# Kernel optimization log

Hardware: AMD Instinct MI355X
Metric: run time of the kernel (lower is better)

Reference implementation:

```python
import jax, jax.numpy as jnp
import numpy as np

N = 50000      # nodes
E = 800000     # edges
IN_CH = 32
H = 64         # hidden_channels
OUT_CH = 16
L = 4          # num_layers
EPS = 1e-7     # GENConv message eps
LN_EPS = 1e-5


def _lin(key, fan_in, fan_out):
    kw, kb = jax.random.split(key)
    s = 1.0 / np.sqrt(fan_in)
    W = jax.random.uniform(kw, (fan_in, fan_out), jnp.float32, -s, s)
    b = jax.random.uniform(kb, (fan_out,), jnp.float32, -s, s)
    return W, b


def setup_inputs() -> dict:
    key = jax.random.key(0)
    ks = jax.random.split(key, 8)
    x = jax.random.normal(ks[0], (N, IN_CH), jnp.float32)
    edge_index = jax.random.randint(ks[1], (2, E), 0, N, dtype=jnp.int32)
    node_W, node_b = _lin(ks[2], IN_CH, H)
    W1, b1, W2, b2 = [], [], [], []
    for i in range(L):
        w1, bb1 = _lin(jax.random.fold_in(ks[3], i), H, 2 * H)
        w2, bb2 = _lin(jax.random.fold_in(ks[4], i), 2 * H, H)
        W1.append(w1); b1.append(bb1); W2.append(w2); b2.append(bb2)
    inp = {
        "x": x,
        "node_W": node_W, "node_b": node_b,
        "W1": jnp.stack(W1), "b1": jnp.stack(b1),          # [L,H,2H],[L,2H]
        "mlp_ln_g": jnp.ones((L, 2 * H), jnp.float32),      # LayerNorm inside GENConv MLP
        "mlp_ln_b": jnp.zeros((L, 2 * H), jnp.float32),
        "W2": jnp.stack(W2), "b2": jnp.stack(b2),          # [L,2H,H],[L,H]
        "t": jnp.ones((L,), jnp.float32),                   # learnable softmax temperature
        "ln_g": jnp.ones((L, H), jnp.float32),              # DeepGCNLayer LayerNorms
        "ln_b": jnp.zeros((L, H), jnp.float32),
        "edge_index": edge_index,
    }
    gW, gb = _lin(ks[5], H, OUT_CH)
    nW, nb = _lin(ks[6], H, OUT_CH + 1)
    inp.update({"g_W": gW, "g_b": gb, "n_W": nW, "n_b": nb})
    return inp


def _layer_norm(h, g, b):
    mu = h.mean(-1, keepdims=True)
    var = ((h - mu) ** 2).mean(-1, keepdims=True)
    return (h - mu) * jax.lax.rsqrt(var + LN_EPS) * g + b


def _gen_conv(h, src, dst, W1, b1, lg, lb, W2, b2, t):
    # message: relu(x_j) + eps  -> [E, H]
    m = jax.nn.relu(h[src]) + EPS
    # per-destination, per-channel scatter softmax with temperature t
    z = t * m
    zmax = jax.ops.segment_max(z, dst, num_segments=N)
    zmax = jnp.where(jnp.isfinite(zmax), zmax, 0.0)  # empty segments -> -inf
    a = jnp.exp(z - zmax[dst])
    denom = jax.ops.segment_sum(a, dst, num_segments=N)
    agg = jax.ops.segment_sum(m * a, dst, num_segments=N) / jnp.maximum(denom, EPS)
    out = agg + h  # root add
    # MLP [H, 2H, H] with LayerNorm + ReLU between
    u = jax.nn.relu(_layer_norm(out @ W1 + b1, lg, lb))
    return u @ W2 + b2


def reference(x, node_W, node_b, W1, b1, mlp_ln_g, mlp_ln_b, W2, b2, t,
              ln_g, ln_b, g_W, g_b, n_W, n_b, edge_index):
    src, dst = edge_index[0], edge_index[1]
    h = x @ node_W + node_b  # node encoder
    # first layer: conv only
    h = _gen_conv(h, src, dst, W1[0], b1[0], mlp_ln_g[0], mlp_ln_b[0], W2[0], b2[0], t[0])
    # remaining res+ blocks: x + conv(relu(norm(x)))  (dropout identity in eval)
    for i in range(1, L):
        y = jax.nn.relu(_layer_norm(h, ln_g[i], ln_b[i]))
        h = h + _gen_conv(y, src, dst, W1[i], b1[i], mlp_ln_g[i], mlp_ln_b[i], W2[i], b2[i], t[i])
    h = jax.nn.relu(_layer_norm(h, ln_g[0], ln_b[0]))
    g_out = jnp.max(h @ g_W + g_b, axis=0)   # batch=None -> global max over nodes
    n_out = h @ n_W + n_b
    return g_out, n_out
```

## Files before the change

### kernel.cpp

```cpp
#include <hip/hip_runtime.h>

#define NN 50000
#define NE 800000
#define INC 32
#define HH 64
#define H2 128
#define OC 16
#define ON 17
#define NL 4
#define MEPS 1e-7f
#define LNE 1e-5f
#define SCAN_BLOCKS 196
#define NOB ((NN + 63) / 64)

typedef __attribute__((ext_vector_type(8))) short bf16x8;
typedef __attribute__((ext_vector_type(4))) float f32x4;

__device__ __forceinline__ unsigned short f2b(float x) {
    unsigned b = __float_as_uint(x);
    b += 0x7FFFu + ((b >> 16) & 1u);
    return (unsigned short)(b >> 16);
}
__device__ __forceinline__ float b2f(unsigned short u) {
    return __uint_as_float(((unsigned)u) << 16);
}

__global__ __launch_bounds__(256) void k_hist2(const int* __restrict__ dst, int* __restrict__ counts,
                                               int* __restrict__ rank) {
    int e = blockIdx.x * 256 + threadIdx.x;
    if (e < NE) rank[e] = atomicAdd(&counts[dst[e]], 1);
}

__global__ __launch_bounds__(256) void k_scan1(const int* __restrict__ counts,
                                               int* __restrict__ incl, int* __restrict__ bsums) {
    __shared__ int s[256];
    int t = threadIdx.x;
    int i = blockIdx.x * 256 + t;
    int v = (i < NN) ? counts[i] : 0;
    s[t] = v;
    __syncthreads();
    for (int off = 1; off < 256; off <<= 1) {
        int x = (t >= off) ? s[t - off] : 0;
        __syncthreads();
        s[t] += x;
        __syncthreads();
    }
    if (i < NN) incl[i] = s[t];
    if (t == 255) bsums[blockIdx.x] = s[255];
}

__global__ __launch_bounds__(256) void k_scan2(int* __restrict__ bsums) {
    __shared__ int s[256];
    int t = threadIdx.x;
    int v = (t < SCAN_BLOCKS) ? bsums[t] : 0;
    s[t] = v;
    __syncthreads();
    for (int off = 1; off < 256; off <<= 1) {
        int x = (t >= off) ? s[t - off] : 0;
        __syncthreads();
        s[t] += x;
        __syncthreads();
    }
    if (t < SCAN_BLOCKS) bsums[t] = s[t] - v;
}

__global__ __launch_bounds__(256) void k_scan3(const int* __restrict__ counts,
                                               int* __restrict__ rowst, const int* __restrict__ bsums,
                                               int2* __restrict__ meta) {
    int i = blockIdx.x * 256 + threadIdx.x;
    if (i < NN) {
        int st = rowst[i] - counts[i] + bsums[blockIdx.x];
        rowst[i] = st;
        meta[i] = make_int2(st, counts[i]);
    }
}

__global__ __launch_bounds__(256) void k_scatter2(const int* __restrict__ src, const int* __restrict__ dst,
                                                  const int* __restrict__ rank, const int* __restrict__ rowst,
                                                  int* __restrict__ ssrc) {
    int e = blockIdx.x * 256 + threadIdx.x;
    if (e < NE) ssrc[rowst[dst[e]] + rank[e]] = src[e];
}

__global__ __launch_bounds__(256) void k_wprep(const float* __restrict__ W1, const float* __restrict__ W2,
                                               const float* __restrict__ nW, const float* __restrict__ gW,
                                               const float* __restrict__ nbp, const float* __restrict__ gb,
                                               unsigned short* __restrict__ w1h, unsigned short* __restrict__ w1l,
                                               unsigned short* __restrict__ w2h, unsigned short* __restrict__ w2l,
                                               unsigned short* __restrict__ whh, unsigned short* __restrict__ whl,
                                               float* __restrict__ bc) {
    int i = blockIdx.x * 256 + threadIdx.x;
    if (i < 48 * 64) {
        int j = i >> 6, k = i & 63;
        float v = 0.f;
        if (j < ON) v = nW[k * ON + j];
        else if (j < 33) v = gW[k * OC + (j - ON)];
        unsigned short hi = f2b(v);
        whh[i] = hi;
        whl[i] = f2b(v - b2f(hi));
    }
    if (i < 48) bc[i] = (i < ON) ? nbp[i] : ((i < 33) ? gb[i - ON] : 0.f);
    if (i >= NL * H2 * HH) return;
    int l = i / (H2 * HH), r = i % (H2 * HH);
    {
        int c = r / HH, k = r % HH;
        float v = W1[(size_t)l * HH * H2 + (size_t)k * H2 + c];
        unsigned short hi = f2b(v);
        w1h[i] = hi;
        w1l[i] = f2b(v - b2f(hi));
    }
    {
        int c = r / H2, k = r % H2;
        float v = W2[(size_t)l * H2 * HH + (size_t)k * HH + c];
        unsigned short hi = f2b(v);
        w2h[i] = hi;
        w2l[i] = f2b(v - b2f(hi));
    }
}

__global__ __launch_bounds__(256) void k_encoder(const float* __restrict__ x, const float* __restrict__ W,
                                                 const float* __restrict__ b, float* __restrict__ h,
                                                 unsigned short* __restrict__ hbf) {
    __shared__ float Ws[INC * HH];
    __shared__ float bs[HH];
    int tid = threadIdx.x;
    for (int i = tid; i < INC * HH; i += 256) Ws[i] = W[i];
    if (tid < HH) bs[tid] = b[tid];
    __syncthreads();
    int wid = tid >> 6, lane = tid & 63;
    int n = blockIdx.x * 4 + wid;
    if (n >= NN) return;
    float v = (lane < INC) ? x[(size_t)n * INC + lane] : 0.f;
    float acc = bs[lane];
    #pragma unroll
    for (int k = 0; k < INC; ++k)
        acc += __shfl(v, k) * Ws[k * HH + lane];
    h[(size_t)n * HH + lane] = acc;
    hbf[(size_t)n * HH + lane] = f2b(acc);
}

__global__ __launch_bounds__(256) void k_agg(const float* __restrict__ y,
                                             const unsigned short* __restrict__ ybf,
                                             const int2* __restrict__ meta,
                                             const int* __restrict__ ssrc,
                                             const float* __restrict__ tp,
                                             unsigned short* __restrict__ agh,
                                             unsigned short* __restrict__ agl) {
    int tid = threadIdx.x;
    int w = tid >> 6, lane = tid & 63;
    int half = lane >> 5;
    int l = lane & 31;
    int col = l;
    int n = blockIdx.x * 8 + w * 2 + half;
    bool valid = n < NN;
    float tval = *tp;
    int2 m = valid ? meta[n] : make_int2(0, 0);
    int start = m.x, deg = m.y;

    int dA = __shfl(deg, 0), dB = __shfl(deg, 32);
    int dmax = max(dA, dB);

    float Sa0 = 0.f, Sm0 = 0.f, Sa1 = 0.f, Sm1 = 0.f;
    for (int win = 0; win < dmax; win += 64) {
        int rem = dmax - win;
        int wcnt = min(64, rem);
        int idxLo = (win + l < deg) ? ssrc[start + win + l] : 0;
        int idxHi = (win + 32 + l < deg) ? ssrc[start + win + 32 + l] : 0;
        for (int e0 = 0; e0 < wcnt; e0 += 8) {
            float c0[8], c1[8];
            int ev[8];
            #pragma unroll
            for (int i = 0; i < 8; ++i) {
                int e = e0 + i;
                ev[i] = win + e;
                int sel = (e < 32) ? idxLo : idxHi;
                int s = __shfl(sel, (lane & 32) | (e & 31));
                unsigned v = *(const unsigned*)(ybf + (size_t)s * HH + col * 2);
                c0[i] = b2f((unsigned short)(v & 0xffffu));
                c1[i] = b2f((unsigned short)(v >> 16));
            }
            #pragma unroll
            for (int i = 0; i < 8; ++i) {
                bool ok = ev[i] < deg;
                float m0 = fmaxf(c0[i], 0.f) + MEPS;
                float m1 = fmaxf(c1[i], 0.f) + MEPS;
                float a0 = ok ? __expf(tval * m0) : 0.f;
                float a1 = ok ? __expf(tval * m1) : 0.f;
                Sa0 += a0; Sm0 += m0 * a0;
                Sa1 += a1; Sm1 += m1 * a1;
            }
        }
    }
    if (!valid) return;
    float agg0 = Sm0 / fmaxf(Sa0, MEPS);
    float agg1 = Sm1 / fmaxf(Sa1, MEPS);
    float2 yv = *(const float2*)(y + (size_t)n * HH + col * 2);
    float av0 = agg0 + yv.x;
    float av1 = agg1 + yv.y;
    unsigned short h0 = f2b(av0), h1 = f2b(av1);
    ushort2 ph = {h0, h1};
    ushort2 pl = {f2b(av0 - b2f(h0)), f2b(av1 - b2f(h1))};
    *(ushort2*)(agh + (size_t)n * HH + col * 2) = ph;
    *(ushort2*)(agl + (size_t)n * HH + col * 2) = pl;
}

__global__ __launch_bounds__(512, 4) void k_mlp(
    const unsigned short* __restrict__ agh, const unsigned short* __restrict__ agl,
    const unsigned short* __restrict__ w1h, const unsigned short* __restrict__ w1l,
    const float* __restrict__ b1,
    const float* __restrict__ mlg, const float* __restrict__ mlb,
    const unsigned short* __restrict__ w2h, const unsigned short* __restrict__ w2l,
    const float* __restrict__ b2,
    const float* __restrict__ hres, float* __restrict__ hout,
    const float* __restrict__ lng1, const float* __restrict__ lnb1,
    float* __restrict__ y, unsigned short* __restrict__ ybf)
{
    __shared__ __align__(16) unsigned short W1S[2 * 128 * 72];
    __shared__ __align__(16) unsigned short W2hS[64 * 136];
    __shared__ __align__(16) unsigned short W2lS[64 * 136];
    int tid = threadIdx.x;
    int w = tid >> 6, lane = tid & 63;
    int nl = lane & 15, g = lane >> 4;
    int node = blockIdx.x * 128 + w * 16 + nl;
    bool valid = node < NN;

    bf16x8 bAh[2], bAl[2];
    {
        bf16x8 z = {0, 0, 0, 0, 0, 0, 0, 0};
        if (valid) {
            const unsigned short* rp = agh + (size_t)node * HH + g * 8;
            bAh[0] = *(const bf16x8*)rp;
            bAh[1] = *(const bf16x8*)(rp + 32);
            const unsigned short* rq = agl + (size_t)node * HH + g * 8;
            bAl[0] = *(const bf16x8*)rq;
            bAl[1] = *(const bf16x8*)(rq + 32);
        } else {
            bAh[0] = z; bAh[1] = z; bAl[0] = z; bAl[1] = z;
        }
    }

    #pragma unroll
    for (int it = 0; it < 2; ++it) {
        int c = tid + it * 512;
        int row = c >> 3, col = (c & 7) << 3;
        float4 vh = *(const float4*)(w1h + c * 8);
        float4 vl = *(const float4*)(w1l + c * 8);
        *(float4*)&W1S[row * 72 + col] = vh;
        *(float4*)&W1S[9216 + row * 72 + col] = vl;
    }
    #pragma unroll
    for (int it = 0; it < 2; ++it) {
        int c = tid + it * 512;
        int row = c >> 4, col = (c & 15) << 3;
        float4 vh = *(const float4*)(w2h + c * 8);
        float4 vl = *(const float4*)(w2l + c * 8);
        *(float4*)&W2hS[row * 136 + col] = vh;
        *(float4*)&W2lS[row * 136 + col] = vl;
    }
    __syncthreads();

    f32x4 accU[8];
    #pragma unroll
    for (int t = 0; t < 8; ++t) {
        int uc = t * 16 + g * 4;
        float4 bb = *(const float4*)(b1 + uc);
        f32x4 a = {bb.x, bb.y, bb.z, bb.w};
        #pragma unroll
        for (int kc = 0; kc < 2; ++kc) {
            int wo = (t * 16 + nl) * 72 + kc * 32 + g * 8;
            bf16x8 ah = *(const bf16x8*)&W1S[wo];
            bf16x8 al = *(const bf16x8*)&W1S[9216 + wo];
            a = __builtin_amdgcn_mfma_f32_16x16x32_bf16(ah, bAh[kc], a, 0, 0, 0);
            a = __builtin_amdgcn_mfma_f32_16x16x32_bf16(al, bAh[kc], a, 0, 0, 0);
            a = __builtin_amdgcn_mfma_f32_16x16x32_bf16(ah, bAl[kc], a, 0, 0, 0);
        }
        accU[t] = a;
    }

    float s = 0.f, sq = 0.f;
    #pragma unroll
    for (int t = 0; t < 8; ++t) {
        #pragma unroll
        for (int j = 0; j < 4; ++j) { float v = accU[t][j]; s += v; sq += v * v; }
    }
    s += __shfl_xor(s, 16); sq += __shfl_xor(sq, 16);
    s += __shfl_xor(s, 32); sq += __shfl_xor(sq, 32);
    float mu = s * (1.f / 128.f);
    float var = sq * (1.f / 128.f) - mu * mu;
    float rs = rsqrtf(fmaxf(var, 0.f) + LNE);

    __syncthreads();
    unsigned short* myUt = W1S + w * (16 * 136);

    #pragma unroll
    for (int t = 0; t < 8; ++t) {
        int uc = t * 16 + g * 4;
        float4 gg = *(const float4*)(mlg + uc);
        float4 bb = *(const float4*)(mlb + uc);
        ushort4 pk;
        pk.x = f2b(fmaxf((accU[t][0] - mu) * rs * gg.x + bb.x, 0.f));
        pk.y = f2b(fmaxf((accU[t][1] - mu) * rs * gg.y + bb.y, 0.f));
        pk.z = f2b(fmaxf((accU[t][2] - mu) * rs * gg.z + bb.z, 0.f));
        pk.w = f2b(fmaxf((accU[t][3] - mu) * rs * gg.w + bb.w, 0.f));
        *(ushort4*)(&myUt[nl * 136 + uc]) = pk;
    }
    asm volatile("s_waitcnt lgkmcnt(0)" ::: "memory");

    bf16x8 bB[4];
    #pragma unroll
    for (int kc = 0; kc < 4; ++kc)
        bB[kc] = *(const bf16x8*)(&myUt[nl * 136 + kc * 32 + g * 8]);

    f32x4 accO[4];
    #pragma unroll
    for (int ot = 0; ot < 4; ++ot) {
        int oc = ot * 16 + g * 4;
        float4 bb = *(const float4*)(b2 + oc);
        f32x4 a = {bb.x, bb.y, bb.z, bb.w};
        #pragma unroll
        for (int kc = 0; kc < 4; ++kc) {
            int wo = (ot * 16 + nl) * 136 + kc * 32 + g * 8;
            bf16x8 ah = *(const bf16x8*)&W2hS[wo];
            bf16x8 al = *(const bf16x8*)&W2lS[wo];
            a = __builtin_amdgcn_mfma_f32_16x16x32_bf16(ah, bB[kc], a, 0, 0, 0);
            a = __builtin_amdgcn_mfma_f32_16x16x32_bf16(al, bB[kc], a, 0, 0, 0);
        }
        accO[ot] = a;
    }

    float4 oo[4];
    #pragma unroll
    for (int ot = 0; ot < 4; ++ot) {
        int oc = ot * 16 + g * 4;
        float4 o;
        o.x = accO[ot][0]; o.y = accO[ot][1]; o.z = accO[ot][2]; o.w = accO[ot][3];
        if (valid) {
            if (hres) {
                float4 hr = *(const float4*)(hres + (size_t)node * HH + oc);
                o.x += hr.x; o.y += hr.y; o.z += hr.z; o.w += hr.w;
            }
            *(float4*)(hout + (size_t)node * HH + oc) = o;
        }
        oo[ot] = o;
    }
    if (!lng1) return;

    float s2 = 0.f, sq2 = 0.f;
    #pragma unroll
    for (int ot = 0; ot < 4; ++ot) {
        s2 += oo[ot].x + oo[ot].y + oo[ot].z + oo[ot].w;
        sq2 += oo[ot].x * oo[ot].x + oo[ot].y * oo[ot].y
             + oo[ot].z * oo[ot].z + oo[ot].w * oo[ot].w;
    }
    s2 += __shfl_xor(s2, 16); sq2 += __shfl_xor(sq2, 16);
    s2 += __shfl_xor(s2, 32); sq2 += __shfl_xor(sq2, 32);
    float mu2 = s2 * (1.f / 64.f);
    float var2 = sq2 * (1.f / 64.f) - mu2 * mu2;
    float rs2 = rsqrtf(fmaxf(var2, 0.f) + LNE);
    #pragma unroll
    for (int ot = 0; ot < 4; ++ot) {
        int oc = ot * 16 + g * 4;
        float4 gg = *(const float4*)(lng1 + oc);
        float4 bb = *(const float4*)(lnb1 + oc);
        float4 v;
        v.x = fmaxf((oo[ot].x - mu2) * rs2 * gg.x + bb.x, 0.f);
        v.y = fmaxf((oo[ot].y - mu2) * rs2 * gg.y + bb.y, 0.f);
        v.z = fmaxf((oo[ot].z - mu2) * rs2 * gg.z + bb.z, 0.f);
        v.w = fmaxf((oo[ot].w - mu2) * rs2 * gg.w + bb.w, 0.f);
        if (valid) {
            *(float4*)(y + (size_t)node * HH + oc) = v;
            ushort4 p;
            p.x = f2b(v.x); p.y = f2b(v.y); p.z = f2b(v.z); p.w = f2b(v.w);
            *(ushort4*)(ybf + (size_t)node * HH + oc) = p;
        }
    }
}

__global__ __launch_bounds__(256) void k_outg(const float* __restrict__ h,
                                              const float* __restrict__ lng, const float* __restrict__ lnb,
                                              const unsigned short* __restrict__ whh,
                                              const unsigned short* __restrict__ whl,
                                              const float* __restrict__ bc,
                                              float* __restrict__ dout, float* __restrict__ gmax) {
    __shared__ float smax[4][16];
    int tid = threadIdx.x;
    int w = tid >> 6, lane = tid & 63;
    int nl = lane & 15, g = lane >> 4;
    int node = blockIdx.x * 64 + w * 16 + nl;
    bool valid = node < NN;

    float hv[16];
    if (valid) {
        const float* hp = h + (size_t)node * HH;
        float4 a0 = *(const float4*)(hp + g * 8);
        float4 a1 = *(const float4*)(hp + g * 8 + 4);
        float4 a2 = *(const float4*)(hp + 32 + g * 8);
        float4 a3 = *(const float4*)(hp + 32 + g * 8 + 4);
        hv[0] = a0.x; hv[1] = a0.y; hv[2] = a0.z; hv[3] = a0.w;
        hv[4] = a1.x; hv[5] = a1.y; hv[6] = a1.z; hv[7] = a1.w;
        hv[8] = a2.x; hv[9] = a2.y; hv[10] = a2.z; hv[11] = a2.w;
        hv[12] = a3.x; hv[13] = a3.y; hv[14] = a3.z; hv[15] = a3.w;
    } else {
        #pragma unroll
        for (int i = 0; i < 16; ++i) hv[i] = 0.f;
    }

    float s = 0.f, sq = 0.f;
    #pragma unroll
    for (int i = 0; i < 16; ++i) { s += hv[i]; sq += hv[i] * hv[i]; }
    s += __shfl_xor(s, 16); sq += __shfl_xor(sq, 16);
    s += __shfl_xor(s, 32); sq += __shfl_xor(sq, 32);
    float mu = s * (1.f / 64.f);
    float var = sq * (1.f / 64.f) - mu * mu;
    float rs = rsqrtf(fmaxf(var, 0.f) + LNE);

    union { bf16x8 v; unsigned short u[8]; } Bh[2], Bl[2];
    #pragma unroll
    for (int kc = 0; kc < 2; ++kc) {
        int cb = kc * 32 + g * 8;
        float4 g0 = *(const float4*)(lng + cb);
        float4 g1 = *(const float4*)(lng + cb + 4);
        float4 b0 = *(const float4*)(lnb + cb);
        float4 b1v = *(const float4*)(lnb + cb + 4);
        float gv[8] = {g0.x, g0.y, g0.z, g0.w, g1.x, g1.y, g1.z, g1.w};
        float bv[8] = {b0.x, b0.y, b0.z, b0.w, b1v.x, b1v.y, b1v.z, b1v.w};
        #pragma unroll
        for (int e = 0; e < 8; ++e) {
            float v = fmaxf((hv[kc * 8 + e] - mu) * rs * gv[e] + bv[e], 0.f);
            unsigned short hi = f2b(v);
            Bh[kc].u[e] = hi;
            Bl[kc].u[e] = f2b(v - b2f(hi));
        }
    }

    f32x4 acc[3];
    #pragma unroll
    for (int t = 0; t < 3; ++t) {
        int j0 = t * 16 + g * 4;
        float4 bb = *(const float4*)(bc + j0);
        f32x4 a = {bb.x, bb.y, bb.z, bb.w};
        #pragma unroll
        for (int kc = 0; kc < 2; ++kc) {
            size_t wo = (size_t)(t * 16 + nl) * 64 + kc * 32 + g * 8;
            bf16x8 ah = *(const bf16x8*)(whh + wo);
            bf16x8 al = *(const bf16x8*)(whl + wo);
            a = __builtin_amdgcn_mfma_f32_16x16x32_bf16(ah, Bh[kc].v, a, 0, 0, 0);
            a = __builtin_amdgcn_mfma_f32_16x16x32_bf16(al, Bh[kc].v, a, 0, 0, 0);
            a = __builtin_amdgcn_mfma_f32_16x16x32_bf16(ah, Bl[kc].v, a, 0, 0, 0);
        }
        acc[t] = a;
    }

    #pragma unroll
    for (int t = 0; t < 3; ++t) {
        #pragma unroll
        for (int reg = 0; reg < 4; ++reg) {
            int j = t * 16 + g * 4 + reg;
            float val = acc[t][reg];
            if (j < ON) {
                if (valid) dout[OC + (size_t)node * ON + j] = val;
            } else if (j < 33) {
                float gv = valid ? val : -INFINITY;
                #pragma unroll
                for (int m = 1; m < 16; m <<= 1) gv = fmaxf(gv, __shfl_xor(gv, m));
                if (nl == 0) smax[w][j - ON] = gv;
            }
        }
    }
    __syncthreads();
    if (tid < 16) {
        float m = fmaxf(fmaxf(smax[0][tid], smax[1][tid]),
                        fmaxf(smax[2][tid], smax[3][tid]));
        gmax[(size_t)blockIdx.x * 16 + tid] = m;
    }
}

__global__ void k_gdec(const float* __restrict__ gmax, float* __restrict__ dout) {
    int lane = threadIdx.x & 63;
    int ch = lane & 15, grp = lane >> 4;
    float m = -INFINITY;
    for (int b = grp; b < NOB; b += 4) m = fmaxf(m, gmax[(size_t)b * 16 + ch]);
    m = fmaxf(m, __shfl_xor(m, 16));
    m = fmaxf(m, __shfl_xor(m, 32));
    if (lane < 16) dout[ch] = m;
}

extern "C" void kernel_launch(void* const* d_in, const int* in_sizes, int n_in,
                              void* d_out, int out_size, void* d_ws, size_t ws_size,
                              hipStream_t stream) {
    const float* x     = (const float*)d_in[0];
    const float* nodeW = (const float*)d_in[1];
    const float* nodeB = (const float*)d_in[2];
    const float* W1    = (const float*)d_in[3];
    const float* b1    = (const float*)d_in[4];
    const float* mlg   = (const float*)d_in[5];
    const float* mlb   = (const float*)d_in[6];
    const float* W2    = (const float*)d_in[7];
    const float* b2    = (const float*)d_in[8];
    const float* tt    = (const float*)d_in[9];
    const float* lng   = (const float*)d_in[10];
    const float* lnb   = (const float*)d_in[11];
    const int*   ei    = (const int*)d_in[12];
    const float* gW    = (const float*)d_in[13];
    const float* gb    = (const float*)d_in[14];
    const float* nW    = (const float*)d_in[15];
    const float* nbp   = (const float*)d_in[16];
    float* out = (float*)d_out;

    char* ws = (char*)d_ws;
    size_t off = 0;
    auto alloc = [&](size_t bytes) -> void* {
        void* p = ws + off;
        off = (off + bytes + 255) & ~(size_t)255;
        return p;
    };
    int* counts    = (int*)alloc((size_t)NN * 4);
    size_t zero_end = off;
    float* gmax = (float*)alloc((size_t)NOB * 16 * 4);
    int* bsums = (int*)alloc(1024);
    int* rowst = (int*)alloc((size_t)NN * 4);
    int2* meta = (int2*)alloc((size_t)NN * 8);
    int* ssrc  = (int*)alloc((size_t)NE * 4);
    float* h   = (float*)alloc((size_t)NN * HH * 4);
    float* y   = (float*)alloc((size_t)NN * HH * 4);
    unsigned short* agh = (unsigned short*)alloc((size_t)NN * HH * 2);
    unsigned short* agl = (unsigned short*)alloc((size_t)NN * HH * 2);
    unsigned short* ybf = (unsigned short*)alloc((size_t)NN * HH * 2);
    unsigned short* w1h = (unsigned short*)alloc((size_t)NL * H2 * HH * 2);
    unsigned short* w1l = (unsigned short*)alloc((size_t)NL * H2 * HH * 2);
    unsigned short* w2h = (unsigned short*)alloc((size_t)NL * H2 * HH * 2);
    unsigned short* w2l = (unsigned short*)alloc((size_t)NL * H2 * HH * 2);
    unsigned short* whh = (unsigned short*)alloc((size_t)48 * 64 * 2);
    unsigned short* whl = (unsigned short*)alloc((size_t)48 * 64 * 2);
    float* bc = (float*)alloc(48 * 4);
    int* rank = (int*)agh;

    const int* esrc = ei;
    const int* edst = ei + NE;

    hipMemsetAsync(d_ws, 0, zero_end, stream);

    k_wprep<<<(NL * H2 * HH + 255) / 256, 256, 0, stream>>>(W1, W2, nW, gW, nbp, gb,
                                                            w1h, w1l, w2h, w2l, whh, whl, bc);
    k_hist2<<<(NE + 255) / 256, 256, 0, stream>>>(edst, counts, rank);
    k_scan1<<<SCAN_BLOCKS, 256, 0, stream>>>(counts, rowst, bsums);
    k_scan2<<<1, 256, 0, stream>>>(bsums);
    k_scan3<<<SCAN_BLOCKS, 256, 0, stream>>>(counts, rowst, bsums, meta);
    k_scatter2<<<(NE + 255) / 256, 256, 0, stream>>>(esrc, edst, rank, rowst, ssrc);
    k_encoder<<<(NN + 3) / 4, 256, 0, stream>>>(x, nodeW, nodeB, h, ybf);

    for (int l = 0; l < NL; ++l) {
        const float* yin = (l == 0) ? h : y;
        k_agg<<<(NN + 7) / 8, 256, 0, stream>>>(yin, ybf, meta, ssrc, tt + l, agh, agl);
        const float* ln1g = (l < NL - 1) ? (lng + (size_t)(l + 1) * HH) : nullptr;
        const float* ln1b = (l < NL - 1) ? (lnb + (size_t)(l + 1) * HH) : nullptr;
        k_mlp<<<(NN + 127) / 128, 512, 0, stream>>>(agh, agl,
                                                    w1h + (size_t)l * H2 * HH, w1l + (size_t)l * H2 * HH,
                                                    b1 + (size_t)l * H2,
                                                    mlg + (size_t)l * H2, mlb + (size_t)l * H2,
                                                    w2h + (size_t)l * H2 * HH, w2l + (size_t)l * H2 * HH,
                                                    b2 + (size_t)l * HH,
                                                    (l == 0) ? (const float*)nullptr : h, h,
                                                    ln1g, ln1b, y, ybf);
    }
    k_outg<<<NOB, 256, 0, stream>>>(h, lng, lnb, whh, whl, bc, out, gmax);
    k_gdec<<<1, 64, 0, stream>>>(gmax, out);
}
```

Baseline: 402.4 us.

## Fuse aggregation, MLP and output head into one per-layer kernel

Merges the weight prep, degree histogram and node encoder into a single multi-role launch, combines scan phases 2 and 3, and fuses the per-layer softmax aggregation into the MLP kernel. The aggregated features now stay in shared memory instead of going to global hi/lo buffers, and the final LayerNorm plus output head runs in the last layer's kernel. The bf16 feature buffer is double-buffered because each layer reads one copy while writing the next. This removes several launches and a global round trip per layer. In exchange, each MLP block of 128 nodes now does the irregular gather itself, which may lower overlap and occupancy and leave the block load uneven.

```diff
diff --git a/kernel.cpp b/kernel.cpp
--- a/kernel.cpp
+++ b/kernel.cpp
@@ -11,7 +11,10 @@
 #define MEPS 1e-7f
 #define LNE 1e-5f
 #define SCAN_BLOCKS 196
-#define NOB ((NN + 63) / 64)
+#define NLB ((NN + 127) / 128)
+#define NBW ((NL * H2 * HH + 255) / 256)
+#define NBH ((NE + 255) / 256)
+#define NBE ((NN + 3) / 4)
 
 typedef __attribute__((ext_vector_type(8))) short bf16x8;
 typedef __attribute__((ext_vector_type(4))) float f32x4;
@@ -25,10 +28,70 @@
     return __uint_as_float(((unsigned)u) << 16);
 }
 
-__global__ __launch_bounds__(256) void k_hist2(const int* __restrict__ dst, int* __restrict__ counts,
-                                               int* __restrict__ rank) {
-    int e = blockIdx.x * 256 + threadIdx.x;
-    if (e < NE) rank[e] = atomicAdd(&counts[dst[e]], 1);
+__global__ __launch_bounds__(256) void k_pre(
+    const float* __restrict__ W1, const float* __restrict__ W2,
+    const float* __restrict__ nW, const float* __restrict__ gW,
+    const float* __restrict__ nbp, const float* __restrict__ gb,
+    unsigned short* __restrict__ w1h, unsigned short* __restrict__ w1l,
+    unsigned short* __restrict__ w2h, unsigned short* __restrict__ w2l,
+    unsigned short* __restrict__ whh, unsigned short* __restrict__ whl,
+    float* __restrict__ bc,
+    const int* __restrict__ edst, int* __restrict__ counts, int* __restrict__ rank,
+    const float* __restrict__ x, const float* __restrict__ nodeW,
+    const float* __restrict__ nodeB, float* __restrict__ h,
+    unsigned short* __restrict__ hbf)
+{
+    __shared__ float Ws[INC * HH];
+    __shared__ float bs[HH];
+    int bid = blockIdx.x, tid = threadIdx.x;
+    if (bid < NBW) {
+        int i = bid * 256 + tid;
+        if (i < 48 * 64) {
+            int j = i >> 6, k = i & 63;
+            float v = 0.f;
+            if (j < ON) v = nW[k * ON + j];
+            else if (j < 33) v = gW[k * OC + (j - ON)];
+            unsigned short hi = f2b(v);
+            whh[i] = hi;
+            whl[i] = f2b(v - b2f(hi));
+        }
+        if (i < 48) bc[i] = (i < ON) ? nbp[i] : ((i < 33) ? gb[i - ON] : 0.f);
+        if (i >= NL * H2 * HH) return;
+        int l = i / (H2 * HH), r = i % (H2 * HH);
+        {
+            int c = r / HH, k = r % HH;
+            float v = W1[(size_t)l * HH * H2 + (size_t)k * H2 + c];
+            unsigned short hi = f2b(v);
+            w1h[i] = hi;
+            w1l[i] = f2b(v - b2f(hi));
+        }
+        {
+            int c = r / H2, k = r % H2;
+            float v = W2[(size_t)l * H2 * HH + (size_t)k * HH + c];
+            unsigned short hi = f2b(v);
+            w2h[i] = hi;
+            w2l[i] = f2b(v - b2f(hi));
+        }
+        return;
+    }
+    if (bid < NBW + NBH) {
+        int e = (bid - NBW) * 256 + tid;
+        if (e < NE) rank[e] = atomicAdd(&counts[edst[e]], 1);
+        return;
+    }
+    for (int i = tid; i < INC * HH; i += 256) Ws[i] = nodeW[i];
+    if (tid < HH) bs[tid] = nodeB[tid];
+    __syncthreads();
+    int wid = tid >> 6, lane = tid & 63;
+    int n = (bid - NBW - NBH) * 4 + wid;
+    if (n >= NN) return;
+    float v = (lane < INC) ? x[(size_t)n * INC + lane] : 0.f;
+    float acc = bs[lane];
+    #pragma unroll
+    for (int k = 0; k < INC; ++k)
+        acc += __shfl(v, k) * Ws[k * HH + lane];
+    h[(size_t)n * HH + lane] = acc;
+    hbf[(size_t)n * HH + lane] = f2b(acc);
 }
 
 __global__ __launch_bounds__(256) void k_scan1(const int* __restrict__ counts,
@@ -49,7 +112,9 @@
     if (t == 255) bsums[blockIdx.x] = s[255];
 }
 
-__global__ __launch_bounds__(256) void k_scan2(int* __restrict__ bsums) {
+__global__ __launch_bounds__(256) void k_scan23(const int* __restrict__ counts,
+                                                int* __restrict__ rowst, const int* __restrict__ bsums,
+                                                int2* __restrict__ meta) {
     __shared__ int s[256];
     int t = threadIdx.x;
     int v = (t < SCAN_BLOCKS) ? bsums[t] : 0;
@@ -61,15 +126,14 @@
         s[t] += x;
         __syncthreads();
     }
-    if (t < SCAN_BLOCKS) bsums[t] = s[t] - v;
-}
-
-__global__ __launch_bounds__(256) void k_scan3(const int* __restrict__ counts,
-                                               int* __restrict__ rowst, const int* __restrict__ bsums,
-                                               int2* __restrict__ meta) {
-    int i = blockIdx.x * 256 + threadIdx.x;
+    int ex = s[t] - v;
+    __syncthreads();
+    s[t] = ex;
+    __syncthreads();
+    int pref = s[blockIdx.x];
+    int i = blockIdx.x * 256 + t;
     if (i < NN) {
-        int st = rowst[i] - counts[i] + bsums[blockIdx.x];
+        int st = rowst[i] - counts[i] + pref;
         rowst[i] = st;
         meta[i] = make_int2(st, counts[i]);
     }
@@ -82,130 +146,9 @@
     if (e < NE) ssrc[rowst[dst[e]] + rank[e]] = src[e];
 }
 
-__global__ __launch_bounds__(256) void k_wprep(const float* __restrict__ W1, const float* __restrict__ W2,
-                                               const float* __restrict__ nW, const float* __restrict__ gW,
-                                               const float* __restrict__ nbp, const float* __restrict__ gb,
-                                               unsigned short* __restrict__ w1h, unsigned short* __restrict__ w1l,
-                                               unsigned short* __restrict__ w2h, unsigned short* __restrict__ w2l,
-                                               unsigned short* __restrict__ whh, unsigned short* __restrict__ whl,
-                                               float* __restrict__ bc) {
-    int i = blockIdx.x * 256 + threadIdx.x;
-    if (i < 48 * 64) {
-        int j = i >> 6, k = i & 63;
-        float v = 0.f;
-        if (j < ON) v = nW[k * ON + j];
-        else if (j < 33) v = gW[k * OC + (j - ON)];
-        unsigned short hi = f2b(v);
-        whh[i] = hi;
-        whl[i] = f2b(v - b2f(hi));
-    }
-    if (i < 48) bc[i] = (i < ON) ? nbp[i] : ((i < 33) ? gb[i - ON] : 0.f);
-    if (i >= NL * H2 * HH) return;
-    int l = i / (H2 * HH), r = i % (H2 * HH);
-    {
-        int c = r / HH, k = r % HH;
-        float v = W1[(size_t)l * HH * H2 + (size_t)k * H2 + c];
-        unsigned short hi = f2b(v);
-        w1h[i] = hi;
-        w1l[i] = f2b(v - b2f(hi));
-    }
-    {
-        int c = r / H2, k = r % H2;
-        float v = W2[(size_t)l * H2 * HH + (size_t)k * HH + c];
-        unsigned short hi = f2b(v);
-        w2h[i] = hi;
-        w2l[i] = f2b(v - b2f(hi));
-    }
-}
-
-__global__ __launch_bounds__(256) void k_encoder(const float* __restrict__ x, const float* __restrict__ W,
-                                                 const float* __restrict__ b, float* __restrict__ h,
-                                                 unsigned short* __restrict__ hbf) {
-    __shared__ float Ws[INC * HH];
-    __shared__ float bs[HH];
-    int tid = threadIdx.x;
-    for (int i = tid; i < INC * HH; i += 256) Ws[i] = W[i];
-    if (tid < HH) bs[tid] = b[tid];
-    __syncthreads();
-    int wid = tid >> 6, lane = tid & 63;
-    int n = blockIdx.x * 4 + wid;
-    if (n >= NN) return;
-    float v = (lane < INC) ? x[(size_t)n * INC + lane] : 0.f;
-    float acc = bs[lane];
-    #pragma unroll
-    for (int k = 0; k < INC; ++k)
-        acc += __shfl(v, k) * Ws[k * HH + lane];
-    h[(size_t)n * HH + lane] = acc;
-    hbf[(size_t)n * HH + lane] = f2b(acc);
-}
-
-__global__ __launch_bounds__(256) void k_agg(const float* __restrict__ y,
-                                             const unsigned short* __restrict__ ybf,
-                                             const int2* __restrict__ meta,
-                                             const int* __restrict__ ssrc,
-                                             const float* __restrict__ tp,
-                                             unsigned short* __restrict__ agh,
-                                             unsigned short* __restrict__ agl) {
-    int tid = threadIdx.x;
-    int w = tid >> 6, lane = tid & 63;
-    int half = lane >> 5;
-    int l = lane & 31;
-    int col = l;
-    int n = blockIdx.x * 8 + w * 2 + half;
-    bool valid = n < NN;
-    float tval = *tp;
-    int2 m = valid ? meta[n] : make_int2(0, 0);
-    int start = m.x, deg = m.y;
-
-    int dA = __shfl(deg, 0), dB = __shfl(deg, 32);
-    int dmax = max(dA, dB);
-
-    float Sa0 = 0.f, Sm0 = 0.f, Sa1 = 0.f, Sm1 = 0.f;
-    for (int win = 0; win < dmax; win += 64) {
-        int rem = dmax - win;
-        int wcnt = min(64, rem);
-        int idxLo = (win + l < deg) ? ssrc[start + win + l] : 0;
-        int idxHi = (win + 32 + l < deg) ? ssrc[start + win + 32 + l] : 0;
-        for (int e0 = 0; e0 < wcnt; e0 += 8) {
-            float c0[8], c1[8];
-            int ev[8];
-            #pragma unroll
-            for (int i = 0; i < 8; ++i) {
-                int e = e0 + i;
-                ev[i] = win + e;
-                int sel = (e < 32) ? idxLo : idxHi;
-                int s = __shfl(sel, (lane & 32) | (e & 31));
-                unsigned v = *(const unsigned*)(ybf + (size_t)s * HH + col * 2);
-                c0[i] = b2f((unsigned short)(v & 0xffffu));
-                c1[i] = b2f((unsigned short)(v >> 16));
-            }
-            #pragma unroll
-            for (int i = 0; i < 8; ++i) {
-                bool ok = ev[i] < deg;
-                float m0 = fmaxf(c0[i], 0.f) + MEPS;
-                float m1 = fmaxf(c1[i], 0.f) + MEPS;
-                float a0 = ok ? __expf(tval * m0) : 0.f;
-                float a1 = ok ? __expf(tval * m1) : 0.f;
-                Sa0 += a0; Sm0 += m0 * a0;
-                Sa1 += a1; Sm1 += m1 * a1;
-            }
-        }
-    }
-    if (!valid) return;
-    float agg0 = Sm0 / fmaxf(Sa0, MEPS);
-    float agg1 = Sm1 / fmaxf(Sa1, MEPS);
-    float2 yv = *(const float2*)(y + (size_t)n * HH + col * 2);
-    float av0 = agg0 + yv.x;
-    float av1 = agg1 + yv.y;
-    unsigned short h0 = f2b(av0), h1 = f2b(av1);
-    ushort2 ph = {h0, h1};
-    ushort2 pl = {f2b(av0 - b2f(h0)), f2b(av1 - b2f(h1))};
-    *(ushort2*)(agh + (size_t)n * HH + col * 2) = ph;
-    *(ushort2*)(agl + (size_t)n * HH + col * 2) = pl;
-}
-
-__global__ __launch_bounds__(512, 4) void k_mlp(
-    const unsigned short* __restrict__ agh, const unsigned short* __restrict__ agl,
+__global__ __launch_bounds__(512, 4) void k_layer(
+    const float* __restrict__ yin, const unsigned short* __restrict__ ybf_in,
+    const int2* __restrict__ meta, const int* __restrict__ ssrc, const float* __restrict__ tp,
     const unsigned short* __restrict__ w1h, const unsigned short* __restrict__ w1l,
     const float* __restrict__ b1,
     const float* __restrict__ mlg, const float* __restrict__ mlb,
@@ -213,31 +156,25 @@
     const float* __restrict__ b2,
     const float* __restrict__ hres, float* __restrict__ hout,
     const float* __restrict__ lng1, const float* __restrict__ lnb1,
-    float* __restrict__ y, unsigned short* __restrict__ ybf)
+    float* __restrict__ yout, unsigned short* __restrict__ ybf_out,
+    const float* __restrict__ lngF, const float* __restrict__ lnbF,
+    const unsigned short* __restrict__ whh, const unsigned short* __restrict__ whl,
+    const float* __restrict__ bc, float* __restrict__ dout, float* __restrict__ gmax)
 {
-    __shared__ __align__(16) unsigned short W1S[2 * 128 * 72];
-    __shared__ __align__(16) unsigned short W2hS[64 * 136];
-    __shared__ __align__(16) unsigned short W2lS[64 * 136];
+    __shared__ __align__(16) unsigned short R1[2 * 128 * 68];
+    __shared__ __align__(16) unsigned short R2[2 * 128 * 72];
+    __shared__ float smax[8][16];
+    unsigned short* aghS = R1;
+    unsigned short* aglS = R1 + 128 * 68;
+    unsigned short* W2hS = R1;
+    unsigned short* W2lS = R1 + 128 * 68;
+    bool last = (lng1 == nullptr);
     int tid = threadIdx.x;
     int w = tid >> 6, lane = tid & 63;
     int nl = lane & 15, g = lane >> 4;
-    int node = blockIdx.x * 128 + w * 16 + nl;
-    bool valid = node < NN;
-
-    bf16x8 bAh[2], bAl[2];
-    {
-        bf16x8 z = {0, 0, 0, 0, 0, 0, 0, 0};
-        if (valid) {
-            const unsigned short* rp = agh + (size_t)node * HH + g * 8;
-            bAh[0] = *(const bf16x8*)rp;
-            bAh[1] = *(const bf16x8*)(rp + 32);
-            const unsigned short* rq = agl + (size_t)node * HH + g * 8;
-            bAl[0] = *(const bf16x8*)rq;
-            bAl[1] = *(const bf16x8*)(rq + 32);
-        } else {
-            bAh[0] = z; bAh[1] = z; bAl[0] = z; bAl[1] = z;
-        }
-    }
+    int nodeM = blockIdx.x * 128 + w * 16 + nl;
+    bool validM = nodeM < NN;
+    float tval = *tp;
 
     #pragma unroll
     for (int it = 0; it < 2; ++it) {
@@ -245,9 +182,104 @@
         int row = c >> 3, col = (c & 7) << 3;
         float4 vh = *(const float4*)(w1h + c * 8);
         float4 vl = *(const float4*)(w1l + c * 8);
-        *(float4*)&W1S[row * 72 + col] = vh;
-        *(float4*)&W1S[9216 + row * 72 + col] = vl;
-    }
+        *(float4*)&R2[row * 72 + col] = vh;
+        *(float4*)&R2[9216 + row * 72 + col] = vl;
+    }
+
+    {
+        int half = lane >> 5, l = lane & 31;
+        for (int p = 0; p < 8; ++p) {
+            int ln = p * 16 + w * 2 + half;
+            int n = blockIdx.x * 128 + ln;
+            bool valid = n < NN;
+            int2 m = valid ? meta[n] : make_int2(0, 0);
+            int start = m.x, deg = m.y;
+            int dA = __shfl(deg, 0), dB = __shfl(deg, 32);
+            int dmax = max(dA, dB);
+            float Sa0 = 0.f, Sm0 = 0.f, Sa1 = 0.f, Sm1 = 0.f;
+            for (int win = 0; win < dmax; win += 64) {
+                int wcnt = min(64, dmax - win);
+                int idxLo = (win + l < deg) ? ssrc[start + win + l] : 0;
+                int idxHi = (win + 32 + l < deg) ? ssrc[start + win + 32 + l] : 0;
+                for (int e0 = 0; e0 < wcnt; e0 += 8) {
+                    float c0[8], c1[8];
+                    int ev[8];
+                    #pragma unroll
+                    for (int i = 0; i < 8; ++i) {
+                        int e = e0 + i;
+                        ev[i] = win + e;
+                        int sel = (e < 32) ? idxLo : idxHi;
+                        int s = __shfl(sel, (lane & 32) | (e & 31));
+                        unsigned vv = *(const unsigned*)(ybf_in + (size_t)s * HH + l * 2);
+                        c0[i] = b2f((unsigned short)(vv & 0xffffu));
+                        c1[i] = b2f((unsigned short)(vv >> 16));
+                    }
+                    #pragma unroll
+                    for (int i = 0; i < 8; ++i) {
+                        bool ok = ev[i] < deg;
+                        float m0 = fmaxf(c0[i], 0.f) + MEPS;
+                        float m1 = fmaxf(c1[i], 0.f) + MEPS;
+                        float a0 = ok ? __expf(tval * m0) : 0.f;
+                        float a1 = ok ? __expf(tval * m1) : 0.f;
+                        Sa0 += a0; Sm0 += m0 * a0;
+                        Sa1 += a1; Sm1 += m1 * a1;
+                    }
+                }
+            }
+            float av0 = 0.f, av1 = 0.f;
+            if (valid) {
+                float2 yv = *(const float2*)(yin + (size_t)n * HH + l * 2);
+                av0 = Sm0 / fmaxf(Sa0, MEPS) + yv.x;
+                av1 = Sm1 / fmaxf(Sa1, MEPS) + yv.y;
+            }
+            unsigned short h0 = f2b(av0), h1 = f2b(av1);
+            ushort2 ph = {h0, h1};
+            ushort2 pl = {f2b(av0 - b2f(h0)), f2b(av1 - b2f(h1))};
+            *(ushort2*)&aghS[ln * 68 + 2 * l] = ph;
+            *(ushort2*)&aglS[ln * 68 + 2 * l] = pl;
+        }
+    }
+    __syncthreads();
+
+    int lnM = w * 16 + nl;
+    bf16x8 bAh[2], bAl[2];
+    #pragma unroll
+    for (int kc = 0; kc < 2; ++kc) {
+        bAh[kc] = *(const bf16x8*)&aghS[lnM * 68 + kc * 32 + g * 8];
+        bAl[kc] = *(const bf16x8*)&aglS[lnM * 68 + kc * 32 + g * 8];
+    }
+    f32x4 accU[8];
+    #pragma unroll
+    for (int t = 0; t < 8; ++t) {
+        int uc = t * 16 + g * 4;
+        float4 bb = *(const float4*)(b1 + uc);
+        f32x4 a = {bb.x, bb.y, bb.z, bb.w};
+        #pragma unroll
+        for (int kc = 0; kc < 2; ++kc) {
+            int wo = (t * 16 + nl) * 72 + kc * 32 + g * 8;
+            bf16x8 ah = *(const bf16x8*)&R2[wo];
+            bf16x8 al = *(const bf16x8*)&R2[9216 + wo];
+            a = __builtin_amdgcn_mfma_f32_16x16x32_bf16(ah, bAh[kc], a, 0, 0, 0);
+            a = __builtin_amdgcn_mfma_f32_16x16x32_bf16(al, bAh[kc], a, 0, 0, 0);
+            a = __builtin_amdgcn_mfma_f32_16x16x32_bf16(ah, bAl[kc], a, 0, 0, 0);
+        }
+        accU[t] = a;
+    }
+
+    float s = 0.f, sq = 0.f;
+    #pragma unroll
+    for (int t = 0; t < 8; ++t) {
+        #pragma unroll
+        for (int j = 0; j < 4; ++j) { float v = accU[t][j]; s += v; sq += v * v; }
+    }
+    s += __shfl_xor(s, 16); sq += __shfl_xor(sq, 16);
+    s += __shfl_xor(s, 32); sq += __shfl_xor(sq, 32);
+    float mu = s * (1.f / 128.f);
+    float var = sq * (1.f / 128.f) - mu * mu;
+    float rs = rsqrtf(fmaxf(var, 0.f) + LNE);
+
+    __syncthreads();
+
     #pragma unroll
     for (int it = 0; it < 2; ++it) {
         int c = tid + it * 512;
@@ -257,41 +289,7 @@
         *(float4*)&W2hS[row * 136 + col] = vh;
         *(float4*)&W2lS[row * 136 + col] = vl;
     }
-    __syncthreads();
-
-    f32x4 accU[8];
-    #pragma unroll
-    for (int t = 0; t < 8; ++t) {
-        int uc = t * 16 + g * 4;
-        float4 bb = *(const float4*)(b1 + uc);
-        f32x4 a = {bb.x, bb.y, bb.z, bb.w};
-        #pragma unroll
-        for (int kc = 0; kc < 2; ++kc) {
-            int wo = (t * 16 + nl) * 72 + kc * 32 + g * 8;
-            bf16x8 ah = *(const bf16x8*)&W1S[wo];
-            bf16x8 al = *(const bf16x8*)&W1S[9216 + wo];
-            a = __builtin_amdgcn_mfma_f32_16x16x32_bf16(ah, bAh[kc], a, 0, 0, 0);
-            a = __builtin_amdgcn_mfma_f32_16x16x32_bf16(al, bAh[kc], a, 0, 0, 0);
-            a = __builtin_amdgcn_mfma_f32_16x16x32_bf16(ah, bAl[kc], a, 0, 0, 0);
-        }
-        accU[t] = a;
-    }
-
-    float s = 0.f, sq = 0.f;
-    #pragma unroll
-    for (int t = 0; t < 8; ++t) {
-        #pragma unroll
-        for (int j = 0; j < 4; ++j) { float v = accU[t][j]; s += v; sq += v * v; }
-    }
-    s += __shfl_xor(s, 16); sq += __shfl_xor(sq, 16);
-    s += __shfl_xor(s, 32); sq += __shfl_xor(sq, 32);
-    float mu = s * (1.f / 128.f);
-    float var = sq * (1.f / 128.f) - mu * mu;
-    float rs = rsqrtf(fmaxf(var, 0.f) + LNE);
-
-    __syncthreads();
-    unsigned short* myUt = W1S + w * (16 * 136);
-
+    unsigned short* myUt = R2 + w * (16 * 136);
     #pragma unroll
     for (int t = 0; t < 8; ++t) {
         int uc = t * 16 + g * 4;
@@ -304,13 +302,12 @@
         pk.w = f2b(fmaxf((accU[t][3] - mu) * rs * gg.w + bb.w, 0.f));
         *(ushort4*)(&myUt[nl * 136 + uc]) = pk;
     }
-    asm volatile("s_waitcnt lgkmcnt(0)" ::: "memory");
+    __syncthreads();
 
     bf16x8 bB[4];
     #pragma unroll
     for (int kc = 0; kc < 4; ++kc)
         bB[kc] = *(const bf16x8*)(&myUt[nl * 136 + kc * 32 + g * 8]);
-
     f32x4 accO[4];
     #pragma unroll
     for (int ot = 0; ot < 4; ++ot) {
@@ -334,16 +331,50 @@
         int oc = ot * 16 + g * 4;
         float4 o;
         o.x = accO[ot][0]; o.y = accO[ot][1]; o.z = accO[ot][2]; o.w = accO[ot][3];
-        if (valid) {
-            if (hres) {
-                float4 hr = *(const float4*)(hres + (size_t)node * HH + oc);
-                o.x += hr.x; o.y += hr.y; o.z += hr.z; o.w += hr.w;
+        if (validM && hres) {
+            float4 hr = *(const float4*)(hres + (size_t)nodeM * HH + oc);
+            o.x += hr.x; o.y += hr.y; o.z += hr.z; o.w += hr.w;
+        }
+        oo[ot] = o;
+    }
+
+    if (!last) {
+        #pragma unroll
+        for (int ot = 0; ot < 4; ++ot) {
+            int oc = ot * 16 + g * 4;
+            if (validM) *(float4*)(hout + (size_t)nodeM * HH + oc) = oo[ot];
+        }
+        float s2 = 0.f, sq2 = 0.f;
+        #pragma unroll
+        for (int ot = 0; ot < 4; ++ot) {
+            s2 += oo[ot].x + oo[ot].y + oo[ot].z + oo[ot].w;
+            sq2 += oo[ot].x * oo[ot].x + oo[ot].y * oo[ot].y
+                 + oo[ot].z * oo[ot].z + oo[ot].w * oo[ot].w;
+        }
+        s2 += __shfl_xor(s2, 16); sq2 += __shfl_xor(sq2, 16);
+        s2 += __shfl_xor(s2, 32); sq2 += __shfl_xor(sq2, 32);
+        float mu2 = s2 * (1.f / 64.f);
+        float var2 = sq2 * (1.f / 64.f) - mu2 * mu2;
+        float rs2 = rsqrtf(fmaxf(var2, 0.f) + LNE);
+        #pragma unroll
+        for (int ot = 0; ot < 4; ++ot) {
+            int oc = ot * 16 + g * 4;
+            float4 gg = *(const float4*)(lng1 + oc);
+            float4 bb = *(const float4*)(lnb1 + oc);
+            float4 v;
+            v.x = fmaxf((oo[ot].x - mu2) * rs2 * gg.x + bb.x, 0.f);
+            v.y = fmaxf((oo[ot].y - mu2) * rs2 * gg.y + bb.y, 0.f);
+            v.z = fmaxf((oo[ot].z - mu2) * rs2 * gg.z + bb.z, 0.f);
+            v.w = fmaxf((oo[ot].w - mu2) * rs2 * gg.w + bb.w, 0.f);
+            if (validM) {
+                *(float4*)(yout + (size_t)nodeM * HH + oc) = v;
+                ushort4 p;
+                p.x = f2b(v.x); p.y = f2b(v.y); p.z = f2b(v.z); p.w = f2b(v.w);
+                *(ushort4*)(ybf_out + (size_t)nodeM * HH + oc) = p;
             }
-            *(float4*)(hout + (size_t)node * HH + oc) = o;
-        }
-        oo[ot] = o;
-    }
-    if (!lng1) return;
+        }
+        return;
+    }
 
     float s2 = 0.f, sq2 = 0.f;
     #pragma unroll
@@ -357,82 +388,21 @@
     float mu2 = s2 * (1.f / 64.f);
     float var2 = sq2 * (1.f / 64.f) - mu2 * mu2;
     float rs2 = rsqrtf(fmaxf(var2, 0.f) + LNE);
-    #pragma unroll
-    for (int ot = 0; ot < 4; ++ot) {
-        int oc = ot * 16 + g * 4;
-        float4 gg = *(const float4*)(lng1 + oc);
-        float4 bb = *(const float4*)(lnb1 + oc);
-        float4 v;
-        v.x = fmaxf((oo[ot].x - mu2) * rs2 * gg.x + bb.x, 0.f);
-        v.y = fmaxf((oo[ot].y - mu2) * rs2 * gg.y + bb.y, 0.f);
-        v.z = fmaxf((oo[ot].z - mu2) * rs2 * gg.z + bb.z, 0.f);
-        v.w = fmaxf((oo[ot].w - mu2) * rs2 * gg.w + bb.w, 0.f);
-        if (valid) {
-            *(float4*)(y + (size_t)node * HH + oc) = v;
-            ushort4 p;
-            p.x = f2b(v.x); p.y = f2b(v.y); p.z = f2b(v.z); p.w = f2b(v.w);
-            *(ushort4*)(ybf + (size_t)node * HH + oc) = p;
-        }
-    }
-}
-
-__global__ __launch_bounds__(256) void k_outg(const float* __restrict__ h,
-                                              const float* __restrict__ lng, const float* __restrict__ lnb,
-                                              const unsigned short* __restrict__ whh,
-                                              const unsigned short* __restrict__ whl,
-                                              const float* __restrict__ bc,
-                                              float* __restrict__ dout, float* __restrict__ gmax) {
-    __shared__ float smax[4][16];
-    int tid = threadIdx.x;
-    int w = tid >> 6, lane = tid & 63;
-    int nl = lane & 15, g = lane >> 4;
-    int node = blockIdx.x * 64 + w * 16 + nl;
-    bool valid = node < NN;
-
-    float hv[16];
-    if (valid) {
-        const float* hp = h + (size_t)node * HH;
-        float4 a0 = *(const float4*)(hp + g * 8);
-        float4 a1 = *(const float4*)(hp + g * 8 + 4);
-        float4 a2 = *(const float4*)(hp + 32 + g * 8);
-        float4 a3 = *(const float4*)(hp + 32 + g * 8 + 4);
-        hv[0] = a0.x; hv[1] = a0.y; hv[2] = a0.z; hv[3] = a0.w;
-        hv[4] = a1.x; hv[5] = a1.y; hv[6] = a1.z; hv[7] = a1.w;
-        hv[8] = a2.x; hv[9] = a2.y; hv[10] = a2.z; hv[11] = a2.w;
-        hv[12] = a3.x; hv[13] = a3.y; hv[14] = a3.z; hv[15] = a3.w;
-    } else {
-        #pragma unroll
-        for (int i = 0; i < 16; ++i) hv[i] = 0.f;
-    }
-
-    float s = 0.f, sq = 0.f;
-    #pragma unroll
-    for (int i = 0; i < 16; ++i) { s += hv[i]; sq += hv[i] * hv[i]; }
-    s += __shfl_xor(s, 16); sq += __shfl_xor(sq, 16);
-    s += __shfl_xor(s, 32); sq += __shfl_xor(sq, 32);
-    float mu = s * (1.f / 64.f);
-    float var = sq * (1.f / 64.f) - mu * mu;
-    float rs = rsqrtf(fmaxf(var, 0.f) + LNE);
 
     union { bf16x8 v; unsigned short u[8]; } Bh[2], Bl[2];
     #pragma unroll
     for (int kc = 0; kc < 2; ++kc) {
-        int cb = kc * 32 + g * 8;
-        float4 g0 = *(const float4*)(lng + cb);
-        float4 g1 = *(const float4*)(lng + cb + 4);
-        float4 b0 = *(const float4*)(lnb + cb);
-        float4 b1v = *(const float4*)(lnb + cb + 4);
-        float gv[8] = {g0.x, g0.y, g0.z, g0.w, g1.x, g1.y, g1.z, g1.w};
-        float bv[8] = {b0.x, b0.y, b0.z, b0.w, b1v.x, b1v.y, b1v.z, b1v.w};
         #pragma unroll
         for (int e = 0; e < 8; ++e) {
-            float v = fmaxf((hv[kc * 8 + e] - mu) * rs * gv[e] + bv[e], 0.f);
+            int ot = kc * 2 + (e >> 2);
+            int c = ot * 16 + g * 4 + (e & 3);
+            float hv = (e & 3) == 0 ? oo[ot].x : ((e & 3) == 1 ? oo[ot].y : ((e & 3) == 2 ? oo[ot].z : oo[ot].w));
+            float v = fmaxf((hv - mu2) * rs2 * lngF[c] + lnbF[c], 0.f);
             unsigned short hi = f2b(v);
             Bh[kc].u[e] = hi;
             Bl[kc].u[e] = f2b(v - b2f(hi));
         }
     }
-
     f32x4 acc[3];
     #pragma unroll
     for (int t = 0; t < 3; ++t) {
@@ -441,12 +411,17 @@
         f32x4 a = {bb.x, bb.y, bb.z, bb.w};
         #pragma unroll
         for (int kc = 0; kc < 2; ++kc) {
-            size_t wo = (size_t)(t * 16 + nl) * 64 + kc * 32 + g * 8;
-            bf16x8 ah = *(const bf16x8*)(whh + wo);
-            bf16x8 al = *(const bf16x8*)(whl + wo);
-            a = __builtin_amdgcn_mfma_f32_16x16x32_bf16(ah, Bh[kc].v, a, 0, 0, 0);
-            a = __builtin_amdgcn_mfma_f32_16x16x32_bf16(al, Bh[kc].v, a, 0, 0, 0);
-            a = __builtin_amdgcn_mfma_f32_16x16x32_bf16(ah, Bl[kc].v, a, 0, 0, 0);
+            union { bf16x8 v; unsigned short u[8]; } Ah, Al;
+            #pragma unroll
+            for (int e = 0; e < 8; ++e) {
+                int ot = kc * 2 + (e >> 2);
+                int c = ot * 16 + g * 4 + (e & 3);
+                Ah.u[e] = whh[(size_t)(t * 16 + nl) * 64 + c];
+                Al.u[e] = whl[(size_t)(t * 16 + nl) * 64 + c];
+            }
+            a = __builtin_amdgcn_mfma_f32_16x16x32_bf16(Ah.v, Bh[kc].v, a, 0, 0, 0);
+            a = __builtin_amdgcn_mfma_f32_16x16x32_bf16(Al.v, Bh[kc].v, a, 0, 0, 0);
+            a = __builtin_amdgcn_mfma_f32_16x16x32_bf16(Ah.v, Bl[kc].v, a, 0, 0, 0);
         }
         acc[t] = a;
     }
@@ -458,9 +433,9 @@
             int j = t * 16 + g * 4 + reg;
             float val = acc[t][reg];
             if (j < ON) {
-                if (valid) dout[OC + (size_t)node * ON + j] = val;
+                if (validM) dout[OC + (size_t)nodeM * ON + j] = val;
             } else if (j < 33) {
-                float gv = valid ? val : -INFINITY;
+                float gv = validM ? val : -INFINITY;
                 #pragma unroll
                 for (int m = 1; m < 16; m <<= 1) gv = fmaxf(gv, __shfl_xor(gv, m));
                 if (nl == 0) smax[w][j - ON] = gv;
@@ -469,9 +444,10 @@
     }
     __syncthreads();
     if (tid < 16) {
-        float m = fmaxf(fmaxf(smax[0][tid], smax[1][tid]),
-                        fmaxf(smax[2][tid], smax[3][tid]));
-        gmax[(size_t)blockIdx.x * 16 + tid] = m;
+        float mm = -INFINITY;
+        #pragma unroll
+        for (int ww = 0; ww < 8; ++ww) mm = fmaxf(mm, smax[ww][tid]);
+        gmax[(size_t)blockIdx.x * 16 + tid] = mm;
     }
 }
 
@@ -479,7 +455,7 @@
     int lane = threadIdx.x & 63;
     int ch = lane & 15, grp = lane >> 4;
     float m = -INFINITY;
-    for (int b = grp; b < NOB; b += 4) m = fmaxf(m, gmax[(size_t)b * 16 + ch]);
+    for (int b = grp; b < NLB; b += 4) m = fmaxf(m, gmax[(size_t)b * 16 + ch]);
     m = fmaxf(m, __shfl_xor(m, 16));
     m = fmaxf(m, __shfl_xor(m, 32));
     if (lane < 16) dout[ch] = m;
@@ -516,16 +492,15 @@
     };
     int* counts    = (int*)alloc((size_t)NN * 4);
     size_t zero_end = off;
-    float* gmax = (float*)alloc((size_t)NOB * 16 * 4);
+    float* gmax = (float*)alloc((size_t)NLB * 16 * 4);
     int* bsums = (int*)alloc(1024);
     int* rowst = (int*)alloc((size_t)NN * 4);
     int2* meta = (int2*)alloc((size_t)NN * 8);
     int* ssrc  = (int*)alloc((size_t)NE * 4);
     float* h   = (float*)alloc((size_t)NN * HH * 4);
     float* y   = (float*)alloc((size_t)NN * HH * 4);
-    unsigned short* agh = (unsigned short*)alloc((size_t)NN * HH * 2);
-    unsigned short* agl = (unsigned short*)alloc((size_t)NN * HH * 2);
-    unsigned short* ybf = (unsigned short*)alloc((size_t)NN * HH * 2);
+    unsigned short* ybf0 = (unsigned short*)alloc((size_t)NN * HH * 2);
+    unsigned short* ybf1 = (unsigned short*)alloc((size_t)NN * HH * 2);
     unsigned short* w1h = (unsigned short*)alloc((size_t)NL * H2 * HH * 2);
     unsigned short* w1l = (unsigned short*)alloc((size_t)NL * H2 * HH * 2);
     unsigned short* w2h = (unsigned short*)alloc((size_t)NL * H2 * HH * 2);
@@ -533,36 +508,38 @@
     unsigned short* whh = (unsigned short*)alloc((size_t)48 * 64 * 2);
     unsigned short* whl = (unsigned short*)alloc((size_t)48 * 64 * 2);
     float* bc = (float*)alloc(48 * 4);
-    int* rank = (int*)agh;
+    int* rank = (int*)ybf1;
 
     const int* esrc = ei;
     const int* edst = ei + NE;
 
     hipMemsetAsync(d_ws, 0, zero_end, stream);
 
-    k_wprep<<<(NL * H2 * HH + 255) / 256, 256, 0, stream>>>(W1, W2, nW, gW, nbp, gb,
-                                                            w1h, w1l, w2h, w2l, whh, whl, bc);
-    k_hist2<<<(NE + 255) / 256, 256, 0, stream>>>(edst, counts, rank);
+    k_pre<<<NBW + NBH + NBE, 256, 0, stream>>>(W1, W2, nW, gW, nbp, gb,
+                                               w1h, w1l, w2h, w2l, whh, whl, bc,
+                                               edst, counts, rank,
+                                               x, nodeW, nodeB, h, ybf0);
     k_scan1<<<SCAN_BLOCKS, 256, 0, stream>>>(counts, rowst, bsums);
-    k_scan2<<<1, 256, 0, stream>>>(bsums);
-    k_scan3<<<SCAN_BLOCKS, 256, 0, stream>>>(counts, rowst, bsums, meta);
+    k_scan23<<<SCAN_BLOCKS, 256, 0, stream>>>(counts, rowst, bsums, meta);
     k_scatter2<<<(NE + 255) / 256, 256, 0, stream>>>(esrc, edst, rank, rowst, ssrc);
-    k_encoder<<<(NN + 3) / 4, 256, 0, stream>>>(x, nodeW, nodeB, h, ybf);
-
+
+    unsigned short* bufs[2] = {ybf0, ybf1};
     for (int l = 0; l < NL; ++l) {
         const float* yin = (l == 0) ? h : y;
-        k_agg<<<(NN + 7) / 8, 256, 0, stream>>>(yin, ybf, meta, ssrc, tt + l, agh, agl);
-        const float* ln1g = (l < NL - 1) ? (lng + (size_t)(l + 1) * HH) : nullptr;
-        const float* ln1b = (l < NL - 1) ? (lnb + (size_t)(l + 1) * HH) : nullptr;
-        k_mlp<<<(NN + 127) / 128, 512, 0, stream>>>(agh, agl,
-                                                    w1h + (size_t)l * H2 * HH, w1l + (size_t)l * H2 * HH,
-                                                    b1 + (size_t)l * H2,
-                                                    mlg + (size_t)l * H2, mlb + (size_t)l * H2,
-                                                    w2h + (size_t)l * H2 * HH, w2l + (size_t)l * H2 * HH,
-                                                    b2 + (size_t)l * HH,
-                                                    (l == 0) ? (const float*)nullptr : h, h,
-                                                    ln1g, ln1b, y, ybf);
-    }
-    k_outg<<<NOB, 256, 0, stream>>>(h, lng, lnb, whh, whl, bc, out, gmax);
+        unsigned short* bin = bufs[l & 1];
+        unsigned short* bout = bufs[(l + 1) & 1];
+        bool lastL = (l == NL - 1);
+        const float* ln1g = lastL ? nullptr : (lng + (size_t)(l + 1) * HH);
+        const float* ln1b = lastL ? nullptr : (lnb + (size_t)(l + 1) * HH);
+        k_layer<<<NLB, 512, 0, stream>>>(yin, bin, meta, ssrc, tt + l,
+                                         w1h + (size_t)l * H2 * HH, w1l + (size_t)l * H2 * HH,
+                                         b1 + (size_t)l * H2,
+                                         mlg + (size_t)l * H2, mlb + (size_t)l * H2,
+                                         w2h + (size_t)l * H2 * HH, w2l + (size_t)l * H2 * HH,
+                                         b2 + (size_t)l * HH,
+                                         (l == 0) ? (const float*)nullptr : h, h,
+                                         ln1g, ln1b, y, bout,
+                                         lng, lnb, whh, whl, bc, out, gmax);
+    }
     k_gdec<<<1, 64, 0, stream>>>(gmax, out);
 }
```

After: 424.3 us. +5.5%, slower.
